# Optimization experiments

Measured on AMD Instinct MI355X. Metric: run time of the kernel, lower is better.

## Reference

```python
import jax, jax.numpy as jnp
import numpy as np

EPS = 1e-6

def _ln2d(x, g, b):
    # x: [b,H,W,c]; LayerNorm2d normalizes over channel dim per spatial location
    mu = jnp.mean(x, axis=-1, keepdims=True)
    var = jnp.mean((x - mu) ** 2, axis=-1, keepdims=True)
    return (x - mu) * jax.lax.rsqrt(var + EPS) * g + b

def _proj(x, w, b):
    # 1x1 conv == channel matmul; w: [c_out, c_in]
    return jnp.einsum('bhwc,dc->bhwd', x, w) + b

def setup_inputs() -> dict:
    key = jax.random.key(0)
    ks = jax.random.split(key, 16)
    b, c, H, W = 8, 96, 128, 256
    s = 0.02
    return {
        'feat_l': jax.random.normal(ks[0], (b, H * W, c), jnp.float32),
        'feat_r': jax.random.normal(ks[1], (b, H * W, c), jnp.float32),
        'g_nl': jnp.ones((c,), jnp.float32),
        'b_nl': jnp.zeros((c,), jnp.float32),
        'g_nr': jnp.ones((c,), jnp.float32),
        'b_nr': jnp.zeros((c,), jnp.float32),
        'w_l1': jax.random.normal(ks[2], (c, c), jnp.float32) * s,
        'bias_l1': jax.random.normal(ks[3], (c,), jnp.float32) * s,
        'w_r1': jax.random.normal(ks[4], (c, c), jnp.float32) * s,
        'bias_r1': jax.random.normal(ks[5], (c,), jnp.float32) * s,
        'w_l2': jax.random.normal(ks[6], (c, c), jnp.float32) * s,
        'bias_l2': jax.random.normal(ks[7], (c,), jnp.float32) * s,
        'w_r2': jax.random.normal(ks[8], (c, c), jnp.float32) * s,
        'bias_r2': jax.random.normal(ks[9], (c,), jnp.float32) * s,
        'beta': jax.random.normal(ks[10], (c,), jnp.float32) * 0.1,
        'gamma': jax.random.normal(ks[11], (c,), jnp.float32) * 0.1,
        'H': 128,
        'W': 256,
    }

def reference(feat_l, feat_r, g_nl, b_nl, g_nr, b_nr,
              w_l1, bias_l1, w_r1, bias_r1, w_l2, bias_l2, w_r2, bias_r2,
              beta, gamma, H, W):
    b, _, c = feat_l.shape
    scale = c ** (-0.5)
    # work in channels-last [b,H,W,c] (equivalent to torch's NCHW + permutes)
    x_l = feat_l.reshape(b, H, W, c)
    x_r = feat_r.reshape(b, H, W, c)
    Q_l = _proj(_ln2d(x_l, g_nl, b_nl), w_l1, bias_l1)   # [b,H,W,c]
    Q_r = _proj(_ln2d(x_r, g_nr, b_nr), w_r1, bias_r1)   # [b,H,W,c]
    V_l = _proj(x_l, w_l2, bias_l2)
    V_r = _proj(x_r, w_r2, bias_r2)
    attn = jnp.einsum('bhwc,bhvc->bhwv', Q_l, Q_r) * scale  # [b,H,W_l,W_r]
    F_r2l = jnp.einsum('bhwv,bhvc->bhwc', jax.nn.softmax(attn, axis=-1), V_r)
    attn_t = jnp.swapaxes(attn, -1, -2)                      # [b,H,W_r,W_l]
    F_l2r = jnp.einsum('bhvw,bhwc->bhvc', jax.nn.softmax(attn_t, axis=-1), V_l)
    out_l = x_l + F_r2l * beta
    out_r = x_r + F_l2r * gamma
    return (out_l.reshape(b, H * W, c), out_r.reshape(b, H * W, c))
```

## Files before the change

kernel.cpp:

```cpp
#include <hip/hip_runtime.h>
#include <stdint.h>

#define C96   96
#define SROWS 256
#define TOTEL 25165824L

typedef __attribute__((ext_vector_type(16))) float f32x16;
typedef __attribute__((ext_vector_type(8)))  short short8;

#define QL_OFF 0
#define QR_OFF 53248
#define SC_OFF 106496
#define XT_OFF SC_OFF
#define VT_OFF (SC_OFF + 13312)
#define ST_OFF 159744
#define LDS_SZ 161792

#define MFMA32(a,b,c) __builtin_amdgcn_mfma_f32_32x32x16_bf16(a,b,c,0,0,0)

__device__ __forceinline__ uint32_t cvtpk(float lo, float hi) {
    uint32_t d;
    asm("v_cvt_pk_bf16_f32 %0, %1, %2" : "=v"(d) : "v"(lo), "v"(hi));
    return d;
}
__device__ __forceinline__ float bl(uint32_t u){ union{uint32_t i;float f;}a; a.i=u<<16;        return a.f; }
__device__ __forceinline__ float bh(uint32_t u){ union{uint32_t i;float f;}a; a.i=u&0xffff0000u; return a.f; }

union F8 { uint32_t u[4]; short8 s; uint4 q; };

template<int ITERS>
__device__ __forceinline__ void stage(const float* __restrict__ src, char* dst, int t) {
#pragma unroll
    for (int i = 0; i < ITERS; ++i) {
        const int idx4 = i * 512 + t;
        const float4 v = *(const float4*)(src + (size_t)idx4 * 4);
        const int r = idx4 / 24;
        const int c = (idx4 % 24) * 4;
        uint2 p; p.x = cvtpk(v.x, v.y); p.y = cvtpk(v.z, v.w);
        *(uint2*)(dst + r * 208 + c * 2) = p;
    }
}

__device__ __forceinline__ void ln_stats(char* lds, int t) {
    if (t < 256) {
        const char* row = lds + SC_OFF + t * 208;
        float sm = 0.f, s2 = 0.f;
#pragma unroll
        for (int i = 0; i < 12; ++i) {
            F8 w; w.q = *(const uint4*)(row + i * 16);
#pragma unroll
            for (int j = 0; j < 4; ++j) {
                const float a = bl(w.u[j]), b = bh(w.u[j]);
                sm += a + b; s2 += a * a + b * b;
            }
        }
        const float mu = sm * (1.f / 96.f);
        float var = s2 * (1.f / 96.f) - mu * mu;
        var = fmaxf(var, 0.f);
        const float rs = rsqrtf(var + 1e-6f);
        *(float2*)(lds + ST_OFF + t * 8) = make_float2(mu, rs);
    }
}

__device__ __forceinline__ void qproj(
    char* lds, char* qdst,
    const float* __restrict__ W1, const float* __restrict__ bias1,
    const float* __restrict__ gv, const float* __restrict__ bv,
    float outscale, int wv, int l31, int s)
{
    const int r = wv * 32 + l31;
    const float2 st = *(const float2*)(lds + ST_OFF + r * 8);
    const float mu = st.x, rs = st.y;
    short8 bfrag[6];
#pragma unroll
    for (int kf = 0; kf < 6; ++kf) {
        const int c0 = kf * 16 + s * 8;
        F8 raw; raw.q = *(const uint4*)(lds + SC_OFF + r * 208 + c0 * 2);
        const float4 g0 = *(const float4*)(gv + c0);
        const float4 g1 = *(const float4*)(gv + c0 + 4);
        const float4 b0 = *(const float4*)(bv + c0);
        const float4 b1 = *(const float4*)(bv + c0 + 4);
        const float x0=bl(raw.u[0]),x1=bh(raw.u[0]),x2=bl(raw.u[1]),x3=bh(raw.u[1]);
        const float x4=bl(raw.u[2]),x5=bh(raw.u[2]),x6=bl(raw.u[3]),x7=bh(raw.u[3]);
        F8 o;
        o.u[0] = cvtpk((x0-mu)*rs*g0.x + b0.x, (x1-mu)*rs*g0.y + b0.y);
        o.u[1] = cvtpk((x2-mu)*rs*g0.z + b0.z, (x3-mu)*rs*g0.w + b0.w);
        o.u[2] = cvtpk((x4-mu)*rs*g1.x + b1.x, (x5-mu)*rs*g1.y + b1.y);
        o.u[3] = cvtpk((x6-mu)*rs*g1.z + b1.z, (x7-mu)*rs*g1.w + b1.w);
        bfrag[kf] = o.s;
    }
    f32x16 qa[3];
#pragma unroll
    for (int i = 0; i < 16; ++i) { qa[0][i] = 0.f; qa[1][i] = 0.f; qa[2][i] = 0.f; }
#pragma unroll
    for (int kf = 0; kf < 6; ++kf) {
        const int cc = kf * 16 + s * 8;
#pragma unroll
        for (int mf = 0; mf < 3; ++mf) {
            const float* wp = W1 + (mf * 32 + l31) * 96 + cc;
            const float4 a0 = *(const float4*)wp;
            const float4 a1 = *(const float4*)(wp + 4);
            F8 af;
            af.u[0] = cvtpk(a0.x, a0.y); af.u[1] = cvtpk(a0.z, a0.w);
            af.u[2] = cvtpk(a1.x, a1.y); af.u[3] = cvtpk(a1.z, a1.w);
            qa[mf] = MFMA32(af.s, bfrag[kf], qa[mf]);
        }
    }
#pragma unroll
    for (int mf = 0; mf < 3; ++mf) {
#pragma unroll
        for (int rq = 0; rq < 4; ++rq) {
            const int d = mf * 32 + rq * 8 + s * 4;
            const float4 bb = *(const float4*)(bias1 + d);
            uint2 p;
            p.x = cvtpk((qa[mf][rq*4+0] + bb.x) * outscale, (qa[mf][rq*4+1] + bb.y) * outscale);
            p.y = cvtpk((qa[mf][rq*4+2] + bb.z) * outscale, (qa[mf][rq*4+3] + bb.w) * outscale);
            *(uint2*)(qdst + r * 208 + d * 2) = p;
        }
    }
}

extern "C" __global__ __launch_bounds__(512, 2) void scam_fused(
    const float* __restrict__ feat_l, const float* __restrict__ feat_r,
    const float* __restrict__ g_nl, const float* __restrict__ b_nl,
    const float* __restrict__ g_nr, const float* __restrict__ b_nr,
    const float* __restrict__ w_l1, const float* __restrict__ bias_l1,
    const float* __restrict__ w_r1, const float* __restrict__ bias_r1,
    const float* __restrict__ w_l2, const float* __restrict__ bias_l2,
    const float* __restrict__ w_r2, const float* __restrict__ bias_r2,
    const float* __restrict__ beta, const float* __restrict__ gamma,
    float* __restrict__ out)
{
    extern __shared__ char lds[];
    const int t    = threadIdx.x;
    const int wv   = t >> 6;
    const int lane = t & 63;
    const int l31  = lane & 31;
    const int s    = lane >> 5;
    const size_t eb = (size_t)blockIdx.x * (SROWS * C96);

    stage<12>(feat_l + eb, lds + SC_OFF, t);
    __syncthreads();
    ln_stats(lds, t);
    __syncthreads();
    qproj(lds, lds + QL_OFF, w_l1, bias_l1, g_nl, b_nl, 0.10206207261596577f, wv, l31, s);
    __syncthreads();
    stage<12>(feat_r + eb, lds + SC_OFF, t);
    __syncthreads();
    ln_stats(lds, t);
    __syncthreads();
    qproj(lds, lds + QR_OFF, w_r1, bias_r1, g_nr, b_nr, 1.0f, wv, l31, s);

    for (int dir = 0; dir < 2; ++dir) {
        const char* Qs = lds + (dir ? QR_OFF : QL_OFF);
        const char* Ks = lds + (dir ? QL_OFF : QR_OFF);
        const float* xv   = dir ? feat_l  : feat_r;
        const float* w2   = dir ? w_l2    : w_r2;
        const float* b2   = dir ? bias_l2 : bias_r2;
        const float* mixv = dir ? gamma   : beta;
        const float* xres = dir ? feat_r  : feat_l;
        float* o = out + (dir ? TOTEL : 0);

        short8 bq[6];
#pragma unroll
        for (int kf = 0; kf < 6; ++kf)
            bq[kf] = *(const short8*)(Qs + (wv * 32 + l31) * 208 + kf * 32 + s * 16);

        short8 wf[6];
        const int mfv = wv % 3, nfv = wv / 3;
        if (wv < 6) {
#pragma unroll
            for (int kf = 0; kf < 6; ++kf) {
                const float* wp = w2 + (mfv * 32 + l31) * 96 + kf * 16 + s * 8;
                const float4 a0 = *(const float4*)wp;
                const float4 a1 = *(const float4*)(wp + 4);
                F8 af;
                af.u[0] = cvtpk(a0.x, a0.y); af.u[1] = cvtpk(a0.z, a0.w);
                af.u[2] = cvtpk(a1.x, a1.y); af.u[3] = cvtpk(a1.z, a1.w);
                wf[kf] = af.s;
            }
        }

        f32x16 O[3];
#pragma unroll
        for (int i = 0; i < 16; ++i) { O[0][i] = 0.f; O[1][i] = 0.f; O[2][i] = 0.f; }
        float m_run = -1e30f, l_run = 0.f;

        __syncthreads();
        stage<3>(xv + eb, lds + XT_OFF, t);

        for (int vt = 0; vt < 4; ++vt) {
            __syncthreads();
            if (wv < 6) {
                f32x16 va;
#pragma unroll
                for (int i = 0; i < 16; ++i) va[i] = 0.f;
#pragma unroll
                for (int kf = 0; kf < 6; ++kf) {
                    const short8 xb = *(const short8*)(lds + XT_OFF + (nfv * 32 + l31) * 208 + kf * 32 + s * 16);
                    va = MFMA32(wf[kf], xb, va);
                }
                const int v = nfv * 32 + l31;
#pragma unroll
                for (int rq = 0; rq < 4; ++rq) {
                    const int d = mfv * 32 + rq * 8 + s * 4;
                    const float4 bb = *(const float4*)(b2 + d);
                    *(uint16_t*)(lds + VT_OFF + (d+0) * 144 + v * 2) = (uint16_t)cvtpk(va[rq*4+0] + bb.x, 0.f);
                    *(uint16_t*)(lds + VT_OFF + (d+1) * 144 + v * 2) = (uint16_t)cvtpk(va[rq*4+1] + bb.y, 0.f);
                    *(uint16_t*)(lds + VT_OFF + (d+2) * 144 + v * 2) = (uint16_t)cvtpk(va[rq*4+2] + bb.z, 0.f);
                    *(uint16_t*)(lds + VT_OFF + (d+3) * 144 + v * 2) = (uint16_t)cvtpk(va[rq*4+3] + bb.w, 0.f);
                }
            }
            __syncthreads();
            if (vt < 3) stage<3>(xv + eb + (size_t)(vt + 1) * 64 * 96, lds + XT_OFF, t);

            f32x16 sa[2];
#pragma unroll
            for (int i = 0; i < 16; ++i) { sa[0][i] = 0.f; sa[1][i] = 0.f; }
#pragma unroll
            for (int kf = 0; kf < 6; ++kf) {
                const short8 a0 = *(const short8*)(Ks + (vt * 64 +      l31) * 208 + kf * 32 + s * 16);
                const short8 a1 = *(const short8*)(Ks + (vt * 64 + 32 + l31) * 208 + kf * 32 + s * 16);
                sa[0] = MFMA32(a0, bq[kf], sa[0]);
                sa[1] = MFMA32(a1, bq[kf], sa[1]);
            }
            float tm = -1e30f;
#pragma unroll
            for (int i = 0; i < 16; ++i) { tm = fmaxf(tm, sa[0][i]); tm = fmaxf(tm, sa[1][i]); }
            tm = fmaxf(tm, __shfl_xor(tm, 32));
            const float mn = fmaxf(m_run, tm);
            const float al = __expf(m_run - mn);
            float ps = 0.f;
#pragma unroll
            for (int i = 0; i < 16; ++i) {
                sa[0][i] = __expf(sa[0][i] - mn); ps += sa[0][i];
                sa[1][i] = __expf(sa[1][i] - mn); ps += sa[1][i];
            }
            ps += __shfl_xor(ps, 32);
            l_run = l_run * al + ps;
            m_run = mn;
            O[0] *= al; O[1] *= al; O[2] *= al;

#pragma unroll
            for (int kk = 0; kk < 4; ++kk) {
                const int mf = kk >> 1, base = (kk & 1) * 8;
                const uint32_t A0 = cvtpk(sa[mf][base+0], sa[mf][base+1]);
                const uint32_t A1 = cvtpk(sa[mf][base+2], sa[mf][base+3]);
                const uint32_t B0 = cvtpk(sa[mf][base+4], sa[mf][base+5]);
                const uint32_t B1 = cvtpk(sa[mf][base+6], sa[mf][base+7]);
                const uint32_t rA0 = __shfl_xor(A0, 32);
                const uint32_t rA1 = __shfl_xor(A1, 32);
                const uint32_t rB0 = __shfl_xor(B0, 32);
                const uint32_t rB1 = __shfl_xor(B1, 32);
                F8 pb;
                pb.u[0] = s ? rB0 : A0;
                pb.u[1] = s ? rB1 : A1;
                pb.u[2] = s ? B0  : rA0;
                pb.u[3] = s ? B1  : rA1;
#pragma unroll
                for (int mf2 = 0; mf2 < 3; ++mf2) {
                    const short8 av = *(const short8*)(lds + VT_OFF + (mf2 * 32 + l31) * 144 + kk * 32 + s * 16);
                    O[mf2] = MFMA32(av, pb.s, O[mf2]);
                }
            }
        }

        const float inv = 1.f / l_run;
        const size_t rowbase = eb + (size_t)(wv * 32 + l31) * 96;
#pragma unroll
        for (int mf = 0; mf < 3; ++mf) {
#pragma unroll
            for (int rq = 0; rq < 4; ++rq) {
                const int d = mf * 32 + rq * 8 + s * 4;
                const float4 mx = *(const float4*)(mixv + d);
                const float4 xr = *(const float4*)(xres + rowbase + d);
                float4 ov;
                ov.x = fmaf(O[mf][rq*4+0] * inv, mx.x, xr.x);
                ov.y = fmaf(O[mf][rq*4+1] * inv, mx.y, xr.y);
                ov.z = fmaf(O[mf][rq*4+2] * inv, mx.z, xr.z);
                ov.w = fmaf(O[mf][rq*4+3] * inv, mx.w, xr.w);
                *(float4*)(o + rowbase + d) = ov;
            }
        }
    }
}

extern "C" void kernel_launch(void* const* d_in, const int* in_sizes, int n_in,
                              void* d_out, int out_size, void* d_ws, size_t ws_size,
                              hipStream_t stream) {
    const float* feat_l  = (const float*)d_in[0];
    const float* feat_r  = (const float*)d_in[1];
    const float* g_nl    = (const float*)d_in[2];
    const float* b_nl    = (const float*)d_in[3];
    const float* g_nr    = (const float*)d_in[4];
    const float* b_nr    = (const float*)d_in[5];
    const float* w_l1    = (const float*)d_in[6];
    const float* bias_l1 = (const float*)d_in[7];
    const float* w_r1    = (const float*)d_in[8];
    const float* bias_r1 = (const float*)d_in[9];
    const float* w_l2    = (const float*)d_in[10];
    const float* bias_l2 = (const float*)d_in[11];
    const float* w_r2    = (const float*)d_in[12];
    const float* bias_r2 = (const float*)d_in[13];
    const float* beta    = (const float*)d_in[14];
    const float* gamma   = (const float*)d_in[15];
    float* out = (float*)d_out;

    hipLaunchKernelGGL(scam_fused, dim3(1024), dim3(512), LDS_SZ, stream,
                       feat_l, feat_r, g_nl, b_nl, g_nr, b_nr,
                       w_l1, bias_l1, w_r1, bias_r1, w_l2, bias_l2, w_r2, bias_r2,
                       beta, gamma, out);
}
```

Baseline: 266.6 us.

## Split attention directions into separate blocks to halve LDS and raise occupancy

Each block now handles one direction of one row slice, so the grid doubles and each block only keeps the key projection in LDS while the query fragments stay in registers via lane shuffles. LDS per block drops to about half, allowing more resident blocks per CU (launch bounds raised to 4). The cost is that both Q projections are recomputed per direction, so LayerNorm and projection work plus input reads are duplicated. Register pressure under the tighter launch bound may cause spills.

```diff
diff --git a/kernel.cpp b/kernel.cpp
--- a/kernel.cpp
+++ b/kernel.cpp
@@ -2,19 +2,16 @@
 #include <stdint.h>
 
 #define C96   96
-#define SROWS 256
 #define TOTEL 25165824L
 
 typedef __attribute__((ext_vector_type(16))) float f32x16;
 typedef __attribute__((ext_vector_type(8)))  short short8;
 
-#define QL_OFF 0
-#define QR_OFF 53248
-#define SC_OFF 106496
-#define XT_OFF SC_OFF
-#define VT_OFF (SC_OFF + 13312)
-#define ST_OFF 159744
-#define LDS_SZ 161792
+#define KQ_OFF 0
+#define SC_OFF 53248
+#define XT_OFF 53248
+#define VT_OFF 66560
+#define LDS_SZ 80384
 
 #define MFMA32(a,b,c) __builtin_amdgcn_mfma_f32_32x32x16_bf16(a,b,c,0,0,0)
 
@@ -41,8 +38,8 @@
     }
 }
 
-__device__ __forceinline__ void ln_stats(char* lds, int t) {
-    if (t < 256) {
+__device__ __forceinline__ void stats128(char* lds, int t) {
+    if (t < 128) {
         const char* row = lds + SC_OFF + t * 208;
         float sm = 0.f, s2 = 0.f;
 #pragma unroll
@@ -57,25 +54,22 @@
         const float mu = sm * (1.f / 96.f);
         float var = s2 * (1.f / 96.f) - mu * mu;
         var = fmaxf(var, 0.f);
-        const float rs = rsqrtf(var + 1e-6f);
-        *(float2*)(lds + ST_OFF + t * 8) = make_float2(mu, rs);
-    }
-}
-
-__device__ __forceinline__ void qproj(
-    char* lds, char* qdst,
-    const float* __restrict__ W1, const float* __restrict__ bias1,
-    const float* __restrict__ gv, const float* __restrict__ bv,
-    float outscale, int wv, int l31, int s)
+        *(float2*)(lds + SC_OFF + t * 208 + 192) = make_float2(mu, rsqrtf(var + 1e-6f));
+    }
+}
+
+__device__ __forceinline__ void proj96(const char* lds_, int rloc,
+    const float* __restrict__ W1, const float* __restrict__ gv,
+    const float* __restrict__ bv, int l31, int s, f32x16* qa)
 {
-    const int r = wv * 32 + l31;
-    const float2 st = *(const float2*)(lds + ST_OFF + r * 8);
+    const char* row = lds_ + SC_OFF + (rloc + l31) * 208;
+    const float2 st = *(const float2*)(row + 192);
     const float mu = st.x, rs = st.y;
-    short8 bfrag[6];
+    short8 bf[6];
 #pragma unroll
     for (int kf = 0; kf < 6; ++kf) {
         const int c0 = kf * 16 + s * 8;
-        F8 raw; raw.q = *(const uint4*)(lds + SC_OFF + r * 208 + c0 * 2);
+        F8 raw; raw.q = *(const uint4*)(row + c0 * 2);
         const float4 g0 = *(const float4*)(gv + c0);
         const float4 g1 = *(const float4*)(gv + c0 + 4);
         const float4 b0 = *(const float4*)(bv + c0);
@@ -87,40 +81,26 @@
         o.u[1] = cvtpk((x2-mu)*rs*g0.z + b0.z, (x3-mu)*rs*g0.w + b0.w);
         o.u[2] = cvtpk((x4-mu)*rs*g1.x + b1.x, (x5-mu)*rs*g1.y + b1.y);
         o.u[3] = cvtpk((x6-mu)*rs*g1.z + b1.z, (x7-mu)*rs*g1.w + b1.w);
-        bfrag[kf] = o.s;
-    }
-    f32x16 qa[3];
+        bf[kf] = o.s;
+    }
 #pragma unroll
     for (int i = 0; i < 16; ++i) { qa[0][i] = 0.f; qa[1][i] = 0.f; qa[2][i] = 0.f; }
 #pragma unroll
     for (int kf = 0; kf < 6; ++kf) {
-        const int cc = kf * 16 + s * 8;
 #pragma unroll
         for (int mf = 0; mf < 3; ++mf) {
-            const float* wp = W1 + (mf * 32 + l31) * 96 + cc;
+            const float* wp = W1 + (mf * 32 + l31) * 96 + kf * 16 + s * 8;
             const float4 a0 = *(const float4*)wp;
             const float4 a1 = *(const float4*)(wp + 4);
             F8 af;
             af.u[0] = cvtpk(a0.x, a0.y); af.u[1] = cvtpk(a0.z, a0.w);
             af.u[2] = cvtpk(a1.x, a1.y); af.u[3] = cvtpk(a1.z, a1.w);
-            qa[mf] = MFMA32(af.s, bfrag[kf], qa[mf]);
-        }
-    }
-#pragma unroll
-    for (int mf = 0; mf < 3; ++mf) {
-#pragma unroll
-        for (int rq = 0; rq < 4; ++rq) {
-            const int d = mf * 32 + rq * 8 + s * 4;
-            const float4 bb = *(const float4*)(bias1 + d);
-            uint2 p;
-            p.x = cvtpk((qa[mf][rq*4+0] + bb.x) * outscale, (qa[mf][rq*4+1] + bb.y) * outscale);
-            p.y = cvtpk((qa[mf][rq*4+2] + bb.z) * outscale, (qa[mf][rq*4+3] + bb.w) * outscale);
-            *(uint2*)(qdst + r * 208 + d * 2) = p;
-        }
-    }
-}
-
-extern "C" __global__ __launch_bounds__(512, 2) void scam_fused(
+            qa[mf] = MFMA32(af.s, bf[kf], qa[mf]);
+        }
+    }
+}
+
+extern "C" __global__ __launch_bounds__(512, 4) void scam_dir(
     const float* __restrict__ feat_l, const float* __restrict__ feat_r,
     const float* __restrict__ g_nl, const float* __restrict__ b_nl,
     const float* __restrict__ g_nr, const float* __restrict__ b_nr,
@@ -137,117 +117,159 @@
     const int lane = t & 63;
     const int l31  = lane & 31;
     const int s    = lane >> 5;
-    const size_t eb = (size_t)blockIdx.x * (SROWS * C96);
-
-    stage<12>(feat_l + eb, lds + SC_OFF, t);
-    __syncthreads();
-    ln_stats(lds, t);
-    __syncthreads();
-    qproj(lds, lds + QL_OFF, w_l1, bias_l1, g_nl, b_nl, 0.10206207261596577f, wv, l31, s);
-    __syncthreads();
-    stage<12>(feat_r + eb, lds + SC_OFF, t);
-    __syncthreads();
-    ln_stats(lds, t);
-    __syncthreads();
-    qproj(lds, lds + QR_OFF, w_r1, bias_r1, g_nr, b_nr, 1.0f, wv, l31, s);
-
-    for (int dir = 0; dir < 2; ++dir) {
-        const char* Qs = lds + (dir ? QR_OFF : QL_OFF);
-        const char* Ks = lds + (dir ? QL_OFF : QR_OFF);
-        const float* xv   = dir ? feat_l  : feat_r;
-        const float* w2   = dir ? w_l2    : w_r2;
-        const float* b2   = dir ? bias_l2 : bias_r2;
-        const float* mixv = dir ? gamma   : beta;
-        const float* xres = dir ? feat_r  : feat_l;
-        float* o = out + (dir ? TOTEL : 0);
-
-        short8 bq[6];
-#pragma unroll
-        for (int kf = 0; kf < 6; ++kf)
-            bq[kf] = *(const short8*)(Qs + (wv * 32 + l31) * 208 + kf * 32 + s * 16);
-
-        short8 wf[6];
-        const int mfv = wv % 3, nfv = wv / 3;
+    const int slice = blockIdx.x >> 1;
+    const int dir   = blockIdx.x & 1;
+    const size_t eb = (size_t)slice * (256 * C96);
+
+    const float* Xq  = dir ? feat_r  : feat_l;
+    const float* Xk  = dir ? feat_l  : feat_r;
+    const float* gq  = dir ? g_nr    : g_nl;
+    const float* bqn = dir ? b_nr    : b_nl;
+    const float* gk  = dir ? g_nl    : g_nr;
+    const float* bkn = dir ? b_nl    : b_nr;
+    const float* W1q = dir ? w_r1    : w_l1;
+    const float* B1q = dir ? bias_r1 : bias_l1;
+    const float* W1k = dir ? w_l1    : w_r1;
+    const float* B1k = dir ? bias_l1 : bias_r1;
+    const float* W2  = dir ? w_l2    : w_r2;
+    const float* B2  = dir ? bias_l2 : bias_r2;
+    const float* mixv = dir ? gamma  : beta;
+    float* o = out + (dir ? TOTEL : 0) + eb;
+
+    short8 bq[6];
+    const float scale = 0.10206207261596577f;
+
+#pragma unroll
+    for (int ch = 0; ch < 2; ++ch) {
+        stage<6>(Xq + eb + (size_t)ch * 128 * 96, lds + SC_OFF, t);
+        __syncthreads();
+        stats128(lds, t);
+        __syncthreads();
+        if ((wv >> 2) == ch) {
+            f32x16 qa[3];
+            proj96(lds, (wv & 3) * 32, W1q, gq, bqn, l31, s, qa);
+#pragma unroll
+            for (int mf = 0; mf < 3; ++mf) {
+                uint32_t w[4][2], x[4][2];
+#pragma unroll
+                for (int blk = 0; blk < 4; ++blk) {
+                    const int d = mf * 32 + blk * 8 + s * 4;
+                    const float4 bb = *(const float4*)(B1q + d);
+                    w[blk][0] = cvtpk((qa[mf][blk*4+0] + bb.x) * scale,
+                                      (qa[mf][blk*4+1] + bb.y) * scale);
+                    w[blk][1] = cvtpk((qa[mf][blk*4+2] + bb.z) * scale,
+                                      (qa[mf][blk*4+3] + bb.w) * scale);
+                    x[blk][0] = __shfl_xor(w[blk][0], 32);
+                    x[blk][1] = __shfl_xor(w[blk][1], 32);
+                }
+#pragma unroll
+                for (int p = 0; p < 2; ++p) {
+                    F8 oo;
+                    oo.u[0] = s ? x[2*p+1][0] : w[2*p][0];
+                    oo.u[1] = s ? x[2*p+1][1] : w[2*p][1];
+                    oo.u[2] = s ? w[2*p+1][0] : x[2*p][0];
+                    oo.u[3] = s ? w[2*p+1][1] : x[2*p][1];
+                    bq[mf*2+p] = oo.s;
+                }
+            }
+        }
+        __syncthreads();
+    }
+#pragma unroll
+    for (int ch = 0; ch < 2; ++ch) {
+        stage<6>(Xk + eb + (size_t)ch * 128 * 96, lds + SC_OFF, t);
+        __syncthreads();
+        stats128(lds, t);
+        __syncthreads();
+        if ((wv >> 2) == ch) {
+            f32x16 qa[3];
+            proj96(lds, (wv & 3) * 32, W1k, gk, bkn, l31, s, qa);
+            const int r = ch * 128 + (wv & 3) * 32 + l31;
+#pragma unroll
+            for (int mf = 0; mf < 3; ++mf) {
+#pragma unroll
+                for (int blk = 0; blk < 4; ++blk) {
+                    const int d = mf * 32 + blk * 8 + s * 4;
+                    const float4 bb = *(const float4*)(B1k + d);
+                    uint2 p;
+                    p.x = cvtpk(qa[mf][blk*4+0] + bb.x, qa[mf][blk*4+1] + bb.y);
+                    p.y = cvtpk(qa[mf][blk*4+2] + bb.z, qa[mf][blk*4+3] + bb.w);
+                    *(uint2*)(lds + KQ_OFF + r * 208 + d * 2) = p;
+                }
+            }
+        }
+        __syncthreads();
+    }
+
+    f32x16 O[3];
+#pragma unroll
+    for (int i = 0; i < 16; ++i) { O[0][i] = 0.f; O[1][i] = 0.f; O[2][i] = 0.f; }
+    float m_run = -1e30f, l_run = 0.f;
+    const int mfv = wv % 3, nfv = wv / 3;
+
+    stage<3>(Xk + eb, lds + XT_OFF, t);
+
+    for (int vt = 0; vt < 4; ++vt) {
+        __syncthreads();
         if (wv < 6) {
+            f32x16 va;
+#pragma unroll
+            for (int i = 0; i < 16; ++i) va[i] = 0.f;
 #pragma unroll
             for (int kf = 0; kf < 6; ++kf) {
-                const float* wp = w2 + (mfv * 32 + l31) * 96 + kf * 16 + s * 8;
+                const float* wp = W2 + (mfv * 32 + l31) * 96 + kf * 16 + s * 8;
                 const float4 a0 = *(const float4*)wp;
                 const float4 a1 = *(const float4*)(wp + 4);
                 F8 af;
                 af.u[0] = cvtpk(a0.x, a0.y); af.u[1] = cvtpk(a0.z, a0.w);
                 af.u[2] = cvtpk(a1.x, a1.y); af.u[3] = cvtpk(a1.z, a1.w);
-                wf[kf] = af.s;
-            }
-        }
-
-        f32x16 O[3];
-#pragma unroll
-        for (int i = 0; i < 16; ++i) { O[0][i] = 0.f; O[1][i] = 0.f; O[2][i] = 0.f; }
-        float m_run = -1e30f, l_run = 0.f;
-
-        __syncthreads();
-        stage<3>(xv + eb, lds + XT_OFF, t);
-
-        for (int vt = 0; vt < 4; ++vt) {
-            __syncthreads();
-            if (wv < 6) {
-                f32x16 va;
-#pragma unroll
-                for (int i = 0; i < 16; ++i) va[i] = 0.f;
-#pragma unroll
-                for (int kf = 0; kf < 6; ++kf) {
-                    const short8 xb = *(const short8*)(lds + XT_OFF + (nfv * 32 + l31) * 208 + kf * 32 + s * 16);
-                    va = MFMA32(wf[kf], xb, va);
-                }
-                const int v = nfv * 32 + l31;
-#pragma unroll
-                for (int rq = 0; rq < 4; ++rq) {
-                    const int d = mfv * 32 + rq * 8 + s * 4;
-                    const float4 bb = *(const float4*)(b2 + d);
-                    *(uint16_t*)(lds + VT_OFF + (d+0) * 144 + v * 2) = (uint16_t)cvtpk(va[rq*4+0] + bb.x, 0.f);
-                    *(uint16_t*)(lds + VT_OFF + (d+1) * 144 + v * 2) = (uint16_t)cvtpk(va[rq*4+1] + bb.y, 0.f);
-                    *(uint16_t*)(lds + VT_OFF + (d+2) * 144 + v * 2) = (uint16_t)cvtpk(va[rq*4+2] + bb.z, 0.f);
-                    *(uint16_t*)(lds + VT_OFF + (d+3) * 144 + v * 2) = (uint16_t)cvtpk(va[rq*4+3] + bb.w, 0.f);
-                }
-            }
-            __syncthreads();
-            if (vt < 3) stage<3>(xv + eb + (size_t)(vt + 1) * 64 * 96, lds + XT_OFF, t);
-
-            f32x16 sa[2];
-#pragma unroll
-            for (int i = 0; i < 16; ++i) { sa[0][i] = 0.f; sa[1][i] = 0.f; }
+                const short8 xb = *(const short8*)(lds + XT_OFF + (nfv * 32 + l31) * 208 + kf * 32 + s * 16);
+                va = MFMA32(af.s, xb, va);
+            }
+            const int v = nfv * 32 + l31;
+#pragma unroll
+            for (int blk = 0; blk < 4; ++blk) {
+                const int d = mfv * 32 + blk * 8 + s * 4;
+                const float4 bb = *(const float4*)(B2 + d);
+                *(uint16_t*)(lds + VT_OFF + (d+0) * 144 + v * 2) = (uint16_t)cvtpk(va[blk*4+0] + bb.x, 0.f);
+                *(uint16_t*)(lds + VT_OFF + (d+1) * 144 + v * 2) = (uint16_t)cvtpk(va[blk*4+1] + bb.y, 0.f);
+                *(uint16_t*)(lds + VT_OFF + (d+2) * 144 + v * 2) = (uint16_t)cvtpk(va[blk*4+2] + bb.z, 0.f);
+                *(uint16_t*)(lds + VT_OFF + (d+3) * 144 + v * 2) = (uint16_t)cvtpk(va[blk*4+3] + bb.w, 0.f);
+            }
+        }
+        __syncthreads();
+        if (vt < 3) stage<3>(Xk + eb + (size_t)(vt + 1) * 64 * 96, lds + XT_OFF, t);
+
+#pragma unroll
+        for (int half = 0; half < 2; ++half) {
+            f32x16 sa;
+#pragma unroll
+            for (int i = 0; i < 16; ++i) sa[i] = 0.f;
 #pragma unroll
             for (int kf = 0; kf < 6; ++kf) {
-                const short8 a0 = *(const short8*)(Ks + (vt * 64 +      l31) * 208 + kf * 32 + s * 16);
-                const short8 a1 = *(const short8*)(Ks + (vt * 64 + 32 + l31) * 208 + kf * 32 + s * 16);
-                sa[0] = MFMA32(a0, bq[kf], sa[0]);
-                sa[1] = MFMA32(a1, bq[kf], sa[1]);
+                const short8 a0 = *(const short8*)(lds + KQ_OFF + (vt * 64 + half * 32 + l31) * 208 + kf * 32 + s * 16);
+                sa = MFMA32(a0, bq[kf], sa);
             }
             float tm = -1e30f;
 #pragma unroll
-            for (int i = 0; i < 16; ++i) { tm = fmaxf(tm, sa[0][i]); tm = fmaxf(tm, sa[1][i]); }
+            for (int i = 0; i < 16; ++i) tm = fmaxf(tm, sa[i]);
             tm = fmaxf(tm, __shfl_xor(tm, 32));
             const float mn = fmaxf(m_run, tm);
             const float al = __expf(m_run - mn);
             float ps = 0.f;
 #pragma unroll
-            for (int i = 0; i < 16; ++i) {
-                sa[0][i] = __expf(sa[0][i] - mn); ps += sa[0][i];
-                sa[1][i] = __expf(sa[1][i] - mn); ps += sa[1][i];
-            }
+            for (int i = 0; i < 16; ++i) { sa[i] = __expf(sa[i] - mn); ps += sa[i]; }
             ps += __shfl_xor(ps, 32);
             l_run = l_run * al + ps;
             m_run = mn;
             O[0] *= al; O[1] *= al; O[2] *= al;
-
-#pragma unroll
-            for (int kk = 0; kk < 4; ++kk) {
-                const int mf = kk >> 1, base = (kk & 1) * 8;
-                const uint32_t A0 = cvtpk(sa[mf][base+0], sa[mf][base+1]);
-                const uint32_t A1 = cvtpk(sa[mf][base+2], sa[mf][base+3]);
-                const uint32_t B0 = cvtpk(sa[mf][base+4], sa[mf][base+5]);
-                const uint32_t B1 = cvtpk(sa[mf][base+6], sa[mf][base+7]);
+#pragma unroll
+            for (int kc = 0; kc < 2; ++kc) {
+                const int base = kc * 8;
+                const uint32_t A0 = cvtpk(sa[base+0], sa[base+1]);
+                const uint32_t A1 = cvtpk(sa[base+2], sa[base+3]);
+                const uint32_t B0 = cvtpk(sa[base+4], sa[base+5]);
+                const uint32_t B1 = cvtpk(sa[base+6], sa[base+7]);
                 const uint32_t rA0 = __shfl_xor(A0, 32);
                 const uint32_t rA1 = __shfl_xor(A1, 32);
                 const uint32_t rB0 = __shfl_xor(B0, 32);
@@ -259,28 +281,28 @@
                 pb.u[3] = s ? B1  : rA1;
 #pragma unroll
                 for (int mf2 = 0; mf2 < 3; ++mf2) {
-                    const short8 av = *(const short8*)(lds + VT_OFF + (mf2 * 32 + l31) * 144 + kk * 32 + s * 16);
+                    const short8 av = *(const short8*)(lds + VT_OFF + (mf2 * 32 + l31) * 144 + half * 64 + kc * 32 + s * 16);
                     O[mf2] = MFMA32(av, pb.s, O[mf2]);
                 }
             }
         }
-
-        const float inv = 1.f / l_run;
-        const size_t rowbase = eb + (size_t)(wv * 32 + l31) * 96;
-#pragma unroll
-        for (int mf = 0; mf < 3; ++mf) {
-#pragma unroll
-            for (int rq = 0; rq < 4; ++rq) {
-                const int d = mf * 32 + rq * 8 + s * 4;
-                const float4 mx = *(const float4*)(mixv + d);
-                const float4 xr = *(const float4*)(xres + rowbase + d);
-                float4 ov;
-                ov.x = fmaf(O[mf][rq*4+0] * inv, mx.x, xr.x);
-                ov.y = fmaf(O[mf][rq*4+1] * inv, mx.y, xr.y);
-                ov.z = fmaf(O[mf][rq*4+2] * inv, mx.z, xr.z);
-                ov.w = fmaf(O[mf][rq*4+3] * inv, mx.w, xr.w);
-                *(float4*)(o + rowbase + d) = ov;
-            }
+    }
+
+    const float inv = 1.f / l_run;
+    const size_t rowbase = eb + (size_t)(wv * 32 + l31) * 96;
+#pragma unroll
+    for (int mf = 0; mf < 3; ++mf) {
+#pragma unroll
+        for (int blk = 0; blk < 4; ++blk) {
+            const int d = mf * 32 + blk * 8 + s * 4;
+            const float4 mx = *(const float4*)(mixv + d);
+            const float4 xr = *(const float4*)(Xq + rowbase + d);
+            float4 ov;
+            ov.x = fmaf(O[mf][blk*4+0] * inv, mx.x, xr.x);
+            ov.y = fmaf(O[mf][blk*4+1] * inv, mx.y, xr.y);
+            ov.z = fmaf(O[mf][blk*4+2] * inv, mx.z, xr.z);
+            ov.w = fmaf(O[mf][blk*4+3] * inv, mx.w, xr.w);
+            *(float4*)(out + (dir ? TOTEL : 0) + rowbase + d) = ov;
         }
     }
 }
@@ -306,7 +328,7 @@
     const float* gamma   = (const float*)d_in[15];
     float* out = (float*)d_out;
 
-    hipLaunchKernelGGL(scam_fused, dim3(1024), dim3(512), LDS_SZ, stream,
+    hipLaunchKernelGGL(scam_dir, dim3(2048), dim3(512), LDS_SZ, stream,
                        feat_l, feat_r, g_nl, b_nl, g_nr, b_nr,
                        w_l1, bias_l1, w_r1, bias_r1, w_l2, bias_l2, w_r2, bias_r2,
                        beta, gamma, out);
```

New measurement: 485.8 us. 1.82x slower.

## Double-buffer V tiles, prefetch scores, stage Q weights in LDS

Applied to the files above, without the earlier changes.

Both feature tiles and both Q-projection weight matrices are loaded into LDS in one pass. LayerNorm statistics are computed for left and right rows together, stored in the row padding, and the projection is written back in place, which removes several barriers. In the attention loop, X/V tiles are double-buffered and the next score tile is computed while the current one goes through softmax, so V projection and staging overlap with the PV MFMAs. The cost is more live accumulator registers under the 512x2 launch bound, which raises the risk of spills.

```diff
diff --git a/kernel.cpp b/kernel.cpp
--- a/kernel.cpp
+++ b/kernel.cpp
@@ -2,19 +2,20 @@
 #include <stdint.h>
 
 #define C96   96
-#define SROWS 256
 #define TOTEL 25165824L
 
 typedef __attribute__((ext_vector_type(16))) float f32x16;
 typedef __attribute__((ext_vector_type(8)))  short short8;
 
-#define QL_OFF 0
-#define QR_OFF 53248
-#define SC_OFF 106496
-#define XT_OFF SC_OFF
-#define VT_OFF (SC_OFF + 13312)
-#define ST_OFF 159744
-#define LDS_SZ 161792
+#define QL_OFF  0
+#define QR_OFF  53248
+#define XT0_OFF 106496
+#define XT1_OFF 119808
+#define VT0_OFF 133120
+#define VT1_OFF 146944
+#define W1Q_OFF 106496
+#define W1K_OFF 126464
+#define LDS_SZ  160768
 
 #define MFMA32(a,b,c) __builtin_amdgcn_mfma_f32_32x32x16_bf16(a,b,c,0,0,0)
 
@@ -41,41 +42,50 @@
     }
 }
 
-__device__ __forceinline__ void ln_stats(char* lds, int t) {
-    if (t < 256) {
-        const char* row = lds + SC_OFF + t * 208;
-        float sm = 0.f, s2 = 0.f;
-#pragma unroll
-        for (int i = 0; i < 12; ++i) {
-            F8 w; w.q = *(const uint4*)(row + i * 16);
-#pragma unroll
-            for (int j = 0; j < 4; ++j) {
-                const float a = bl(w.u[j]), b = bh(w.u[j]);
-                sm += a + b; s2 += a * a + b * b;
-            }
-        }
-        const float mu = sm * (1.f / 96.f);
-        float var = s2 * (1.f / 96.f) - mu * mu;
-        var = fmaxf(var, 0.f);
-        const float rs = rsqrtf(var + 1e-6f);
-        *(float2*)(lds + ST_OFF + t * 8) = make_float2(mu, rs);
-    }
-}
-
-__device__ __forceinline__ void qproj(
-    char* lds, char* qdst,
-    const float* __restrict__ W1, const float* __restrict__ bias1,
+__device__ __forceinline__ void stageW(const float* __restrict__ W, char* dst, int t) {
+#pragma unroll
+    for (int i = 0; i < 5; ++i) {
+        const int idx4 = i * 512 + t;
+        if (idx4 < 2304) {
+            const float4 v = *(const float4*)(W + (size_t)idx4 * 4);
+            const int r = idx4 / 24;
+            const int c = (idx4 % 24) * 4;
+            uint2 p; p.x = cvtpk(v.x, v.y); p.y = cvtpk(v.z, v.w);
+            *(uint2*)(dst + r * 208 + c * 2) = p;
+        }
+    }
+}
+
+__device__ __forceinline__ void stats512(char* lds_, int t) {
+    char* row = lds_ + ((t < 256) ? QL_OFF : QR_OFF) + (t & 255) * 208;
+    float sm = 0.f, s2 = 0.f;
+#pragma unroll
+    for (int i = 0; i < 12; ++i) {
+        F8 w; w.q = *(const uint4*)(row + i * 16);
+#pragma unroll
+        for (int j = 0; j < 4; ++j) {
+            const float a = bl(w.u[j]), b = bh(w.u[j]);
+            sm += a + b; s2 += a * a + b * b;
+        }
+    }
+    const float mu = sm * (1.f / 96.f);
+    float var = s2 * (1.f / 96.f) - mu * mu;
+    var = fmaxf(var, 0.f);
+    *(float2*)(row + 192) = make_float2(mu, rsqrtf(var + 1e-6f));
+}
+
+__device__ __forceinline__ void proj_inplace(char* lds_, int qoff, int woff,
     const float* __restrict__ gv, const float* __restrict__ bv,
-    float outscale, int wv, int l31, int s)
+    const float* __restrict__ bias1, float outscale, int wv, int l31, int s)
 {
-    const int r = wv * 32 + l31;
-    const float2 st = *(const float2*)(lds + ST_OFF + r * 8);
+    char* row = lds_ + qoff + (wv * 32 + l31) * 208;
+    const float2 st = *(const float2*)(row + 192);
     const float mu = st.x, rs = st.y;
-    short8 bfrag[6];
+    short8 bf[6];
 #pragma unroll
     for (int kf = 0; kf < 6; ++kf) {
         const int c0 = kf * 16 + s * 8;
-        F8 raw; raw.q = *(const uint4*)(lds + SC_OFF + r * 208 + c0 * 2);
+        F8 raw; raw.q = *(const uint4*)(row + c0 * 2);
         const float4 g0 = *(const float4*)(gv + c0);
         const float4 g1 = *(const float4*)(gv + c0 + 4);
         const float4 b0 = *(const float4*)(bv + c0);
@@ -87,36 +97,67 @@
         o.u[1] = cvtpk((x2-mu)*rs*g0.z + b0.z, (x3-mu)*rs*g0.w + b0.w);
         o.u[2] = cvtpk((x4-mu)*rs*g1.x + b1.x, (x5-mu)*rs*g1.y + b1.y);
         o.u[3] = cvtpk((x6-mu)*rs*g1.z + b1.z, (x7-mu)*rs*g1.w + b1.w);
-        bfrag[kf] = o.s;
+        bf[kf] = o.s;
     }
     f32x16 qa[3];
 #pragma unroll
     for (int i = 0; i < 16; ++i) { qa[0][i] = 0.f; qa[1][i] = 0.f; qa[2][i] = 0.f; }
 #pragma unroll
     for (int kf = 0; kf < 6; ++kf) {
-        const int cc = kf * 16 + s * 8;
 #pragma unroll
         for (int mf = 0; mf < 3; ++mf) {
-            const float* wp = W1 + (mf * 32 + l31) * 96 + cc;
-            const float4 a0 = *(const float4*)wp;
-            const float4 a1 = *(const float4*)(wp + 4);
-            F8 af;
-            af.u[0] = cvtpk(a0.x, a0.y); af.u[1] = cvtpk(a0.z, a0.w);
-            af.u[2] = cvtpk(a1.x, a1.y); af.u[3] = cvtpk(a1.z, a1.w);
-            qa[mf] = MFMA32(af.s, bfrag[kf], qa[mf]);
+            const short8 af = *(const short8*)(lds_ + woff + (mf * 32 + l31) * 208 + kf * 32 + s * 16);
+            qa[mf] = MFMA32(af, bf[kf], qa[mf]);
         }
     }
 #pragma unroll
     for (int mf = 0; mf < 3; ++mf) {
 #pragma unroll
-        for (int rq = 0; rq < 4; ++rq) {
-            const int d = mf * 32 + rq * 8 + s * 4;
+        for (int blk = 0; blk < 4; ++blk) {
+            const int d = mf * 32 + blk * 8 + s * 4;
             const float4 bb = *(const float4*)(bias1 + d);
             uint2 p;
-            p.x = cvtpk((qa[mf][rq*4+0] + bb.x) * outscale, (qa[mf][rq*4+1] + bb.y) * outscale);
-            p.y = cvtpk((qa[mf][rq*4+2] + bb.z) * outscale, (qa[mf][rq*4+3] + bb.w) * outscale);
-            *(uint2*)(qdst + r * 208 + d * 2) = p;
-        }
+            p.x = cvtpk((qa[mf][blk*4+0] + bb.x) * outscale, (qa[mf][blk*4+1] + bb.y) * outscale);
+            p.y = cvtpk((qa[mf][blk*4+2] + bb.z) * outscale, (qa[mf][blk*4+3] + bb.w) * outscale);
+            *(uint2*)(row + d * 2) = p;
+        }
+    }
+}
+
+__device__ __forceinline__ void vproj(char* lds_, int xt_off, int vt_off,
+    const short8* wf, const float* __restrict__ B2, int mfv, int nfv, int l31, int s)
+{
+    f32x16 va;
+#pragma unroll
+    for (int i = 0; i < 16; ++i) va[i] = 0.f;
+#pragma unroll
+    for (int kf = 0; kf < 6; ++kf) {
+        const short8 xb = *(const short8*)(lds_ + xt_off + (nfv * 32 + l31) * 208 + kf * 32 + s * 16);
+        va = MFMA32(wf[kf], xb, va);
+    }
+    const int v = nfv * 32 + l31;
+#pragma unroll
+    for (int blk = 0; blk < 4; ++blk) {
+        const int d = mfv * 32 + blk * 8 + s * 4;
+        const float4 bb = *(const float4*)(B2 + d);
+        *(uint16_t*)(lds_ + vt_off + (d+0) * 144 + v * 2) = (uint16_t)cvtpk(va[blk*4+0] + bb.x, 0.f);
+        *(uint16_t*)(lds_ + vt_off + (d+1) * 144 + v * 2) = (uint16_t)cvtpk(va[blk*4+1] + bb.y, 0.f);
+        *(uint16_t*)(lds_ + vt_off + (d+2) * 144 + v * 2) = (uint16_t)cvtpk(va[blk*4+2] + bb.z, 0.f);
+        *(uint16_t*)(lds_ + vt_off + (d+3) * 144 + v * 2) = (uint16_t)cvtpk(va[blk*4+3] + bb.w, 0.f);
+    }
+}
+
+__device__ __forceinline__ void scalc(const char* lds_, int koff, int vt,
+                                      const short8* bq, int l31, int s, f32x16* sa)
+{
+#pragma unroll
+    for (int i = 0; i < 16; ++i) { sa[0][i] = 0.f; sa[1][i] = 0.f; }
+#pragma unroll
+    for (int kf = 0; kf < 6; ++kf) {
+        const short8 a0 = *(const short8*)(lds_ + koff + (vt * 64 +      l31) * 208 + kf * 32 + s * 16);
+        const short8 a1 = *(const short8*)(lds_ + koff + (vt * 64 + 32 + l31) * 208 + kf * 32 + s * 16);
+        sa[0] = MFMA32(a0, bq[kf], sa[0]);
+        sa[1] = MFMA32(a1, bq[kf], sa[1]);
     }
 }
 
@@ -137,41 +178,39 @@
     const int lane = t & 63;
     const int l31  = lane & 31;
     const int s    = lane >> 5;
-    const size_t eb = (size_t)blockIdx.x * (SROWS * C96);
-
-    stage<12>(feat_l + eb, lds + SC_OFF, t);
+    const size_t eb = (size_t)blockIdx.x * (256 * C96);
+    const float scale = 0.10206207261596577f;
+
+    stage<12>(feat_l + eb, lds + QL_OFF, t);
+    stage<12>(feat_r + eb, lds + QR_OFF, t);
+    stageW(w_l1, lds + (0 ? W1K_OFF : W1Q_OFF), t);
+    stageW(w_r1, lds + W1K_OFF, t);
     __syncthreads();
-    ln_stats(lds, t);
+    stats512(lds, t);
     __syncthreads();
-    qproj(lds, lds + QL_OFF, w_l1, bias_l1, g_nl, b_nl, 0.10206207261596577f, wv, l31, s);
-    __syncthreads();
-    stage<12>(feat_r + eb, lds + SC_OFF, t);
-    __syncthreads();
-    ln_stats(lds, t);
-    __syncthreads();
-    qproj(lds, lds + QR_OFF, w_r1, bias_r1, g_nr, b_nr, 1.0f, wv, l31, s);
+    proj_inplace(lds, QL_OFF, W1Q_OFF, g_nl, b_nl, bias_l1, scale, wv, l31, s);
+    proj_inplace(lds, QR_OFF, W1K_OFF, g_nr, b_nr, bias_r1, 1.0f,  wv, l31, s);
 
     for (int dir = 0; dir < 2; ++dir) {
-        const char* Qs = lds + (dir ? QR_OFF : QL_OFF);
-        const char* Ks = lds + (dir ? QL_OFF : QR_OFF);
-        const float* xv   = dir ? feat_l  : feat_r;
-        const float* w2   = dir ? w_l2    : w_r2;
-        const float* b2   = dir ? bias_l2 : bias_r2;
+        const int qoff = dir ? QR_OFF : QL_OFF;
+        const int koff = dir ? QL_OFF : QR_OFF;
+        const float* Xk   = dir ? feat_l  : feat_r;
+        const float* Xq   = dir ? feat_r  : feat_l;
+        const float* W2   = dir ? w_l2    : w_r2;
+        const float* B2   = dir ? bias_l2 : bias_r2;
         const float* mixv = dir ? gamma   : beta;
-        const float* xres = dir ? feat_r  : feat_l;
-        float* o = out + (dir ? TOTEL : 0);
 
         short8 bq[6];
 #pragma unroll
         for (int kf = 0; kf < 6; ++kf)
-            bq[kf] = *(const short8*)(Qs + (wv * 32 + l31) * 208 + kf * 32 + s * 16);
+            bq[kf] = *(const short8*)(lds + qoff + (wv * 32 + l31) * 208 + kf * 32 + s * 16);
 
         short8 wf[6];
         const int mfv = wv % 3, nfv = wv / 3;
         if (wv < 6) {
 #pragma unroll
             for (int kf = 0; kf < 6; ++kf) {
-                const float* wp = w2 + (mfv * 32 + l31) * 96 + kf * 16 + s * 8;
+                const float* wp = W2 + (mfv * 32 + l31) * 96 + kf * 16 + s * 8;
                 const float4 a0 = *(const float4*)wp;
                 const float4 a1 = *(const float4*)(wp + 4);
                 F8 af;
@@ -185,45 +224,22 @@
 #pragma unroll
         for (int i = 0; i < 16; ++i) { O[0][i] = 0.f; O[1][i] = 0.f; O[2][i] = 0.f; }
         float m_run = -1e30f, l_run = 0.f;
+        f32x16 sab[2][2];
 
         __syncthreads();
-        stage<3>(xv + eb, lds + XT_OFF, t);
-
+        stage<3>(Xk + eb, lds + XT0_OFF, t);
+        __syncthreads();
+        if (wv < 6) vproj(lds, XT0_OFF, VT0_OFF, wf, B2, mfv, nfv, l31, s);
+        stage<3>(Xk + eb + 64 * 96, lds + XT1_OFF, t);
+        __syncthreads();
+        scalc(lds, koff, 0, bq, l31, s, sab[0]);
+
+#pragma unroll
         for (int vt = 0; vt < 4; ++vt) {
-            __syncthreads();
-            if (wv < 6) {
-                f32x16 va;
-#pragma unroll
-                for (int i = 0; i < 16; ++i) va[i] = 0.f;
-#pragma unroll
-                for (int kf = 0; kf < 6; ++kf) {
-                    const short8 xb = *(const short8*)(lds + XT_OFF + (nfv * 32 + l31) * 208 + kf * 32 + s * 16);
-                    va = MFMA32(wf[kf], xb, va);
-                }
-                const int v = nfv * 32 + l31;
-#pragma unroll
-                for (int rq = 0; rq < 4; ++rq) {
-                    const int d = mfv * 32 + rq * 8 + s * 4;
-                    const float4 bb = *(const float4*)(b2 + d);
-                    *(uint16_t*)(lds + VT_OFF + (d+0) * 144 + v * 2) = (uint16_t)cvtpk(va[rq*4+0] + bb.x, 0.f);
-                    *(uint16_t*)(lds + VT_OFF + (d+1) * 144 + v * 2) = (uint16_t)cvtpk(va[rq*4+1] + bb.y, 0.f);
-                    *(uint16_t*)(lds + VT_OFF + (d+2) * 144 + v * 2) = (uint16_t)cvtpk(va[rq*4+2] + bb.z, 0.f);
-                    *(uint16_t*)(lds + VT_OFF + (d+3) * 144 + v * 2) = (uint16_t)cvtpk(va[rq*4+3] + bb.w, 0.f);
-                }
-            }
-            __syncthreads();
-            if (vt < 3) stage<3>(xv + eb + (size_t)(vt + 1) * 64 * 96, lds + XT_OFF, t);
-
-            f32x16 sa[2];
-#pragma unroll
-            for (int i = 0; i < 16; ++i) { sa[0][i] = 0.f; sa[1][i] = 0.f; }
-#pragma unroll
-            for (int kf = 0; kf < 6; ++kf) {
-                const short8 a0 = *(const short8*)(Ks + (vt * 64 +      l31) * 208 + kf * 32 + s * 16);
-                const short8 a1 = *(const short8*)(Ks + (vt * 64 + 32 + l31) * 208 + kf * 32 + s * 16);
-                sa[0] = MFMA32(a0, bq[kf], sa[0]);
-                sa[1] = MFMA32(a1, bq[kf], sa[1]);
-            }
+            const int cb = vt & 1, nb = cb ^ 1;
+            if (vt < 3) scalc(lds, koff, vt + 1, bq, l31, s, sab[nb]);
+
+            f32x16* sa = sab[cb];
             float tm = -1e30f;
 #pragma unroll
             for (int i = 0; i < 16; ++i) { tm = fmaxf(tm, sa[0][i]); tm = fmaxf(tm, sa[1][i]); }
@@ -241,6 +257,7 @@
             m_run = mn;
             O[0] *= al; O[1] *= al; O[2] *= al;
 
+            const int vtoff = cb ? VT1_OFF : VT0_OFF;
 #pragma unroll
             for (int kk = 0; kk < 4; ++kk) {
                 const int mf = kk >> 1, base = (kk & 1) * 8;
@@ -259,27 +276,37 @@
                 pb.u[3] = s ? B1  : rA1;
 #pragma unroll
                 for (int mf2 = 0; mf2 < 3; ++mf2) {
-                    const short8 av = *(const short8*)(lds + VT_OFF + (mf2 * 32 + l31) * 144 + kk * 32 + s * 16);
+                    const short8 av = *(const short8*)(lds + vtoff + (mf2 * 32 + l31) * 144 + kk * 32 + s * 16);
                     O[mf2] = MFMA32(av, pb.s, O[mf2]);
                 }
             }
+
+            if (vt < 3) {
+                __syncthreads();
+                if (wv < 6) vproj(lds, nb ? XT1_OFF : XT0_OFF, nb ? VT1_OFF : VT0_OFF,
+                                  wf, B2, mfv, nfv, l31, s);
+                if (vt < 2) stage<3>(Xk + eb + (size_t)(vt + 2) * 64 * 96,
+                                     lds + (cb ? XT1_OFF : XT0_OFF), t);
+                __syncthreads();
+            }
         }
 
         const float inv = 1.f / l_run;
         const size_t rowbase = eb + (size_t)(wv * 32 + l31) * 96;
+        float* oo = out + (dir ? TOTEL : 0);
 #pragma unroll
         for (int mf = 0; mf < 3; ++mf) {
 #pragma unroll
-            for (int rq = 0; rq < 4; ++rq) {
-                const int d = mf * 32 + rq * 8 + s * 4;
+            for (int blk = 0; blk < 4; ++blk) {
+                const int d = mf * 32 + blk * 8 + s * 4;
                 const float4 mx = *(const float4*)(mixv + d);
-                const float4 xr = *(const float4*)(xres + rowbase + d);
+                const float4 xr = *(const float4*)(Xq + rowbase + d);
                 float4 ov;
-                ov.x = fmaf(O[mf][rq*4+0] * inv, mx.x, xr.x);
-                ov.y = fmaf(O[mf][rq*4+1] * inv, mx.y, xr.y);
-                ov.z = fmaf(O[mf][rq*4+2] * inv, mx.z, xr.z);
-                ov.w = fmaf(O[mf][rq*4+3] * inv, mx.w, xr.w);
-                *(float4*)(o + rowbase + d) = ov;
+                ov.x = fmaf(O[mf][blk*4+0] * inv, mx.x, xr.x);
+                ov.y = fmaf(O[mf][blk*4+1] * inv, mx.y, xr.y);
+                ov.z = fmaf(O[mf][blk*4+2] * inv, mx.z, xr.z);
+                ov.w = fmaf(O[mf][blk*4+3] * inv, mx.w, xr.w);
+                *(float4*)(oo + rowbase + d) = ov;
             }
         }
     }
```

Result: faster. 215.2 us (-19.3%).
